# Kernel optimization log

Measured on AMD Instinct MI355X. Metric: run time of the kernel, lower is better.

The kernel has to match this reference:

```python
import jax, jax.numpy as jnp
import numpy as np

B, D, H, S = 65536, 256, 4, 64
HD = D // H  # head_dim = 64
EPS = 1e-8


def _lin(x, W, b):
    # torch nn.Linear: y = x @ W.T + b, W: [out, in]
    return x @ W.T + b


def _cos_attn(q_heads, keys, vals):
    # q_heads: [B,H,hd]; keys/vals: [H,S,hd] (shared across batch)
    qn = q_heads / (jnp.linalg.norm(q_heads, axis=-1, keepdims=True) + EPS)
    kn = keys / (jnp.linalg.norm(keys, axis=-1, keepdims=True) + EPS)
    sim = jnp.einsum('bhd,hsd->bhs', qn, kn)          # cosine sims, temp=1.0
    attn = jax.nn.softmax(sim, axis=-1)
    return jnp.einsum('bhs,hsd->bhd', attn, vals)     # [B,H,hd]


def setup_inputs() -> dict:
    key = jax.random.key(0)
    ks = jax.random.split(key, 20)

    def xavier(k, shape):
        fan_in, fan_out = shape[1], shape[0]
        lim = np.sqrt(6.0 / (fan_in + fan_out))
        return jax.random.uniform(k, shape, jnp.float32, -lim, lim)

    return {
        'query': jax.random.normal(ks[0], (B, D), jnp.float32),
        'context': jax.random.normal(ks[1], (B, D), jnp.float32),
        'fast_keys': 0.01 * jax.random.normal(ks[2], (H, S, HD), jnp.float32),
        'fast_vals': 0.01 * jax.random.normal(ks[3], (H, S, HD), jnp.float32),
        'deep_keys': 0.01 * jax.random.normal(ks[4], (H, S, HD), jnp.float32),
        'deep_vals': 0.01 * jax.random.normal(ks[5], (H, S, HD), jnp.float32),
        'Wq': xavier(ks[6], (D, D)), 'bq': jnp.zeros((D,), jnp.float32),
        'Wg': xavier(ks[7], (D, D)), 'bg': jnp.zeros((D,), jnp.float32),
        'Wc1': xavier(ks[8], (D // 2, D)), 'bc1': jnp.zeros((D // 2,), jnp.float32),
        'Wc2': xavier(ks[9], (1, D // 2)), 'bc2': jnp.zeros((1,), jnp.float32),
        'Wo': xavier(ks[10], (D, D)), 'bo': jnp.zeros((D,), jnp.float32),
        'Ws': xavier(ks[11], (D, D)), 'bs': jnp.zeros((D,), jnp.float32),
        'mix_logit': jnp.zeros((), jnp.float32),
        'surprise_mean': jnp.zeros((1, D), jnp.float32),
        'surprise_var': jnp.ones((1, D), jnp.float32),
    }


def reference(query, context, fast_keys, fast_vals, deep_keys, deep_vals,
              Wq, bq, Wg, bg, Wc1, bc1, Wc2, bc2, Wo, bo, Ws, bs,
              mix_logit, surprise_mean, surprise_var):
    # --- query projection and head split ---
    q = _lin(query, Wq, bq)                       # [B, D]
    q_heads = q.reshape(B, H, HD)                 # [B, H, hd]

    # --- dual-tier cosine-similarity attention reads ---
    v_fast = _cos_attn(q_heads, fast_keys, fast_vals).reshape(B, D)
    v_deep = _cos_attn(q_heads, deep_keys, deep_vals).reshape(B, D)

    # --- context-gated mixing of tiers ---
    gate = jnp.tanh(_lin(context, Wg, bg)).mean(axis=-1, keepdims=True)  # [B,1]
    mix = jax.nn.sigmoid(mix_logit + gate)
    out = mix * v_fast + (1.0 - mix) * v_deep

    # --- adaptive retrieval confidence head ---
    conf = jax.nn.sigmoid(_lin(jnp.tanh(_lin(context, Wc1, bc1)), Wc2, bc2))  # [B,1]
    out = out * conf
    out = _lin(out, Wo, bo)                       # [B, d_value]

    # --- surprise (detached diagnostic, does not feed output) ---
    h = jax.lax.stop_gradient(_lin(context, Ws, bs))
    z = (h - surprise_mean) / jnp.sqrt(surprise_var + 1e-6)
    surprise = jax.nn.sigmoid(jnp.abs(z).mean(axis=-1) - 2.0)  # 1/max(0.5,0.1)=2.0
    del surprise  # aux diagnostic; main output is the retrieved vector
    return out
```

## Files before the change

### kernel.cpp

```cpp
#include <hip/hip_runtime.h>

typedef unsigned short u16;
typedef __attribute__((ext_vector_type(8))) short bf16x8;
typedef __attribute__((ext_vector_type(4))) float f32x4;
typedef __attribute__((ext_vector_type(4))) unsigned short u16x4;

#define MFMA16(a, b, c) __builtin_amdgcn_mfma_f32_16x16x32_bf16((a), (b), (c), 0, 0, 0)

#define OFF_WQ   0
#define OFF_WG   65536
#define OFF_WC1  131072
#define OFF_WO   163840
#define OFF_KNF  229376
#define OFF_VTF  245760
#define OFF_KND  262144
#define OFF_VTD  278528

__device__ __forceinline__ u16 f2b(float f) {
  union { float f; unsigned u; } v; v.f = f;
  unsigned r = v.u + 0x7fffu + ((v.u >> 16) & 1u);
  return (u16)(r >> 16);
}
__device__ __forceinline__ float fsig(float x) {
  return __builtin_amdgcn_rcpf(1.f + __expf(-x));
}
__device__ __forceinline__ float ftanh(float x) {
  float e = __expf(2.f * x);
  return (e - 1.f) * __builtin_amdgcn_rcpf(e + 1.f);
}
__device__ __forceinline__ float sum16(float v) {
  v += __shfl_xor(v, 1);
  v += __shfl_xor(v, 2);
  v += __shfl_xor(v, 4);
  v += __shfl_xor(v, 8);
  return v;
}
__device__ __forceinline__ float sum64(float v) {
  v += __shfl_xor(v, 1);
  v += __shfl_xor(v, 2);
  v += __shfl_xor(v, 4);
  v += __shfl_xor(v, 8);
  v += __shfl_xor(v, 16);
  v += __shfl_xor(v, 32);
  return v;
}

__global__ void k_convert(const float* __restrict__ Wq, const float* __restrict__ Wg,
                          const float* __restrict__ Wc1, const float* __restrict__ Wo,
                          u16* __restrict__ ws) {
  int i = blockIdx.x * 256 + threadIdx.x;
  ws[OFF_WQ + i] = f2b(Wq[i]);
  ws[OFF_WG + i] = f2b(Wg[i]);
  ws[OFF_WO + i] = f2b(Wo[i]);
  if (i < 32768) ws[OFF_WC1 + i] = f2b(Wc1[i]);
}

__global__ void k_prep(const float* __restrict__ fk, const float* __restrict__ fv,
                       const float* __restrict__ dk, const float* __restrict__ dv,
                       u16* __restrict__ ws) {
  int t = blockIdx.x;
  int h = t >> 6, s = t & 63;
  int d = threadIdx.x;

  float x = fk[t * 64 + d];
  float ss = sum64(x * x);
  float sc = __builtin_amdgcn_rcpf(__builtin_amdgcn_sqrtf(ss) + 1e-8f);
  ws[OFF_KNF + t * 64 + d] = f2b(x * sc);

  x = dk[t * 64 + d];
  ss = sum64(x * x);
  sc = __builtin_amdgcn_rcpf(__builtin_amdgcn_sqrtf(ss) + 1e-8f);
  ws[OFF_KND + t * 64 + d] = f2b(x * sc);

  ws[OFF_VTF + h * 4096 + d * 64 + s] = f2b(fv[t * 64 + d]);
  ws[OFF_VTD + h * 4096 + d * 64 + s] = f2b(dv[t * 64 + d]);
}

__global__ __launch_bounds__(256, 4)
void k_fused(const float* __restrict__ query, const float* __restrict__ context,
             const float* __restrict__ bq, const float* __restrict__ bg,
             const float* __restrict__ bc1, const float* __restrict__ Wc2,
             const float* __restrict__ bc2v, const float* __restrict__ bo,
             const float* __restrict__ mixl, const u16* __restrict__ ws,
             float* __restrict__ outp) {
  __shared__ u16 sX[32 * 256];
  __shared__ float red_g[4][32];
  __shared__ float red_c[4][32];
  __shared__ float sA[32];
  __shared__ float sB[32];

  const int t = threadIdx.x;
  const int w = t >> 6;
  const int lane = t & 63;
  const int quad = lane >> 4;
  const int l16 = lane & 15;
  const int row4 = quad * 4;
  const int blk = blockIdx.x;
  char* Xb = (char*)sX;
  char* chunk = Xb + w * 4096;

  auto stage = [&](const float* src) {
    #pragma unroll
    for (int i = 0; i < 8; ++i) {
      int e = i * 1024 + t * 4;
      float4 v = *(const float4*)(src + e);
      int row = e >> 8, col = e & 255;
      u16x4 pk;
      pk.x = f2b(v.x); pk.y = f2b(v.y); pk.z = f2b(v.z); pk.w = f2b(v.w);
      *(u16x4*)(Xb + row * 512 + ((((col >> 3) ^ (row & 7)) << 4) | ((col & 7) << 1))) = pk;
    }
  };
  auto ldA = [&](int row, int kb) {
    return *(const bf16x8*)(Xb + row * 512 + ((((kb >> 3) ^ (row & 7)) << 4)));
  };
  auto ldC = [&](int row, int kb) {
    return *(const bf16x8*)(chunk + row * 128 + ((((kb >> 3) ^ (row & 7)) << 4)));
  };
  auto cwr = [&](int row, int col, u16 v) {
    *(u16*)(chunk + row * 128 + (((((col >> 3) ^ (row & 7)) << 3) | (col & 7)) << 1)) = v;
  };

  const f32x4 vzero = {0.f, 0.f, 0.f, 0.f};

  stage(context + (size_t)blk * 8192);
  __syncthreads();

  {
    f32x4 acc[2][4];
    #pragma unroll
    for (int mt = 0; mt < 2; ++mt)
      #pragma unroll
      for (int nt = 0; nt < 4; ++nt) acc[mt][nt] = vzero;
    const u16* WB = ws + OFF_WG + (w * 64 + l16) * 256;
    #pragma unroll
    for (int kk = 0; kk < 8; ++kk) {
      int kb = kk * 32 + quad * 8;
      bf16x8 a0 = ldA(l16, kb), a1 = ldA(16 + l16, kb);
      #pragma unroll
      for (int nt = 0; nt < 4; ++nt) {
        bf16x8 b = *(const bf16x8*)(WB + nt * 4096 + kb);
        acc[0][nt] = MFMA16(a0, b, acc[0][nt]);
        acc[1][nt] = MFMA16(a1, b, acc[1][nt]);
      }
    }
    float bgv[4];
    #pragma unroll
    for (int nt = 0; nt < 4; ++nt) bgv[nt] = bg[w * 64 + nt * 16 + l16];
    #pragma unroll
    for (int mt = 0; mt < 2; ++mt)
      #pragma unroll
      for (int r = 0; r < 4; ++r) {
        float s = 0.f;
        #pragma unroll
        for (int nt = 0; nt < 4; ++nt) s += ftanh(acc[mt][nt][r] + bgv[nt]);
        s = sum16(s);
        if (l16 == 0) red_g[w][mt * 16 + row4 + r] = s;
      }
  }
  {
    f32x4 acc[2][2];
    #pragma unroll
    for (int mt = 0; mt < 2; ++mt) { acc[mt][0] = vzero; acc[mt][1] = vzero; }
    const u16* WB = ws + OFF_WC1 + (w * 32 + l16) * 256;
    #pragma unroll
    for (int kk = 0; kk < 8; ++kk) {
      int kb = kk * 32 + quad * 8;
      bf16x8 a0 = ldA(l16, kb), a1 = ldA(16 + l16, kb);
      #pragma unroll
      for (int nt = 0; nt < 2; ++nt) {
        bf16x8 b = *(const bf16x8*)(WB + nt * 4096 + kb);
        acc[0][nt] = MFMA16(a0, b, acc[0][nt]);
        acc[1][nt] = MFMA16(a1, b, acc[1][nt]);
      }
    }
    float bcv[2], wcv[2];
    #pragma unroll
    for (int nt = 0; nt < 2; ++nt) {
      int n = w * 32 + nt * 16 + l16;
      bcv[nt] = bc1[n]; wcv[nt] = Wc2[n];
    }
    #pragma unroll
    for (int mt = 0; mt < 2; ++mt)
      #pragma unroll
      for (int r = 0; r < 4; ++r) {
        float s = 0.f;
        #pragma unroll
        for (int nt = 0; nt < 2; ++nt) s += ftanh(acc[mt][nt][r] + bcv[nt]) * wcv[nt];
        s = sum16(s);
        if (l16 == 0) red_c[w][mt * 16 + row4 + r] = s;
      }
  }
  __syncthreads();
  if (t < 32) {
    float g = (red_g[0][t] + red_g[1][t] + red_g[2][t] + red_g[3][t]) * (1.f / 256.f);
    float mix = fsig(mixl[0] + g);
    float conf = fsig(red_c[0][t] + red_c[1][t] + red_c[2][t] + red_c[3][t] + bc2v[0]);
    sA[t] = conf * mix;
    sB[t] = conf - conf * mix;
  }
  __syncthreads();

  stage(query + (size_t)blk * 8192);
  __syncthreads();

  f32x4 qa[2][4];
  {
    #pragma unroll
    for (int mt = 0; mt < 2; ++mt)
      #pragma unroll
      for (int nt = 0; nt < 4; ++nt) qa[mt][nt] = vzero;
    const u16* WB = ws + OFF_WQ + (w * 64 + l16) * 256;
    #pragma unroll
    for (int kk = 0; kk < 8; ++kk) {
      int kb = kk * 32 + quad * 8;
      bf16x8 a0 = ldA(l16, kb), a1 = ldA(16 + l16, kb);
      #pragma unroll
      for (int nt = 0; nt < 4; ++nt) {
        bf16x8 b = *(const bf16x8*)(WB + nt * 4096 + kb);
        qa[0][nt] = MFMA16(a0, b, qa[0][nt]);
        qa[1][nt] = MFMA16(a1, b, qa[1][nt]);
      }
    }
    float bqv[4];
    #pragma unroll
    for (int nt = 0; nt < 4; ++nt) bqv[nt] = bq[w * 64 + nt * 16 + l16];
    #pragma unroll
    for (int mt = 0; mt < 2; ++mt)
      #pragma unroll
      for (int nt = 0; nt < 4; ++nt)
        #pragma unroll
        for (int r = 0; r < 4; ++r) qa[mt][nt][r] += bqv[nt];
  }
  float scl[2][4];
  #pragma unroll
  for (int mt = 0; mt < 2; ++mt)
    #pragma unroll
    for (int r = 0; r < 4; ++r) {
      float ss = 0.f;
      #pragma unroll
      for (int nt = 0; nt < 4; ++nt) ss += qa[mt][nt][r] * qa[mt][nt][r];
      ss = sum16(ss);
      scl[mt][r] = __builtin_amdgcn_rcpf(__builtin_amdgcn_sqrtf(ss) + 1e-8f);
    }
  __syncthreads();

  #pragma unroll
  for (int mt = 0; mt < 2; ++mt)
    #pragma unroll
    for (int r = 0; r < 4; ++r) {
      int row = mt * 16 + row4 + r;
      #pragma unroll
      for (int nt = 0; nt < 4; ++nt)
        cwr(row, nt * 16 + l16, f2b(qa[mt][nt][r] * scl[mt][r]));
    }

  f32x4 sf[2][4], sd[2][4];
  #pragma unroll
  for (int mt = 0; mt < 2; ++mt)
    #pragma unroll
    for (int nt = 0; nt < 4; ++nt) { sf[mt][nt] = vzero; sd[mt][nt] = vzero; }
  {
    const u16* knF = ws + OFF_KNF + w * 4096;
    const u16* knD = ws + OFF_KND + w * 4096;
    #pragma unroll
    for (int kk = 0; kk < 2; ++kk) {
      int kb = kk * 32 + quad * 8;
      bf16x8 a0 = ldC(l16, kb), a1 = ldC(16 + l16, kb);
      #pragma unroll
      for (int nt = 0; nt < 4; ++nt) {
        bf16x8 bF = *(const bf16x8*)(knF + (nt * 16 + l16) * 64 + kb);
        bf16x8 bD = *(const bf16x8*)(knD + (nt * 16 + l16) * 64 + kb);
        sf[0][nt] = MFMA16(a0, bF, sf[0][nt]);
        sf[1][nt] = MFMA16(a1, bF, sf[1][nt]);
        sd[0][nt] = MFMA16(a0, bD, sd[0][nt]);
        sd[1][nt] = MFMA16(a1, bD, sd[1][nt]);
      }
    }
  }

  f32x4 oacc[2][4];
  {
    #pragma unroll
    for (int mt = 0; mt < 2; ++mt)
      #pragma unroll
      for (int r = 0; r < 4; ++r) {
        float rs = 0.f;
        #pragma unroll
        for (int nt = 0; nt < 4; ++nt) { float e = __expf(sf[mt][nt][r]); sf[mt][nt][r] = e; rs += e; }
        rs = sum16(rs);
        float inv = __builtin_amdgcn_rcpf(rs);
        int row = mt * 16 + row4 + r;
        #pragma unroll
        for (int nt = 0; nt < 4; ++nt) cwr(row, nt * 16 + l16, f2b(sf[mt][nt][r] * inv));
      }
    f32x4 pv[2][4];
    #pragma unroll
    for (int mt = 0; mt < 2; ++mt)
      #pragma unroll
      for (int nt = 0; nt < 4; ++nt) pv[mt][nt] = vzero;
    const u16* vT = ws + OFF_VTF + w * 4096;
    #pragma unroll
    for (int kk = 0; kk < 2; ++kk) {
      int kb = kk * 32 + quad * 8;
      bf16x8 a0 = ldC(l16, kb), a1 = ldC(16 + l16, kb);
      #pragma unroll
      for (int nt = 0; nt < 4; ++nt) {
        bf16x8 b = *(const bf16x8*)(vT + (nt * 16 + l16) * 64 + kb);
        pv[0][nt] = MFMA16(a0, b, pv[0][nt]);
        pv[1][nt] = MFMA16(a1, b, pv[1][nt]);
      }
    }
    #pragma unroll
    for (int mt = 0; mt < 2; ++mt)
      #pragma unroll
      for (int r = 0; r < 4; ++r) {
        float m_ = sA[mt * 16 + row4 + r];
        #pragma unroll
        for (int nt = 0; nt < 4; ++nt) oacc[mt][nt][r] = m_ * pv[mt][nt][r];
      }
  }
  {
    #pragma unroll
    for (int mt = 0; mt < 2; ++mt)
      #pragma unroll
      for (int r = 0; r < 4; ++r) {
        float rs = 0.f;
        #pragma unroll
        for (int nt = 0; nt < 4; ++nt) { float e = __expf(sd[mt][nt][r]); sd[mt][nt][r] = e; rs += e; }
        rs = sum16(rs);
        float inv = __builtin_amdgcn_rcpf(rs);
        int row = mt * 16 + row4 + r;
        #pragma unroll
        for (int nt = 0; nt < 4; ++nt) cwr(row, nt * 16 + l16, f2b(sd[mt][nt][r] * inv));
      }
    f32x4 pv[2][4];
    #pragma unroll
    for (int mt = 0; mt < 2; ++mt)
      #pragma unroll
      for (int nt = 0; nt < 4; ++nt) pv[mt][nt] = vzero;
    const u16* vT = ws + OFF_VTD + w * 4096;
    #pragma unroll
    for (int kk = 0; kk < 2; ++kk) {
      int kb = kk * 32 + quad * 8;
      bf16x8 a0 = ldC(l16, kb), a1 = ldC(16 + l16, kb);
      #pragma unroll
      for (int nt = 0; nt < 4; ++nt) {
        bf16x8 b = *(const bf16x8*)(vT + (nt * 16 + l16) * 64 + kb);
        pv[0][nt] = MFMA16(a0, b, pv[0][nt]);
        pv[1][nt] = MFMA16(a1, b, pv[1][nt]);
      }
    }
    #pragma unroll
    for (int mt = 0; mt < 2; ++mt)
      #pragma unroll
      for (int r = 0; r < 4; ++r) {
        float m_ = sB[mt * 16 + row4 + r];
        #pragma unroll
        for (int nt = 0; nt < 4; ++nt) oacc[mt][nt][r] += m_ * pv[mt][nt][r];
      }
  }

  __syncthreads();
  #pragma unroll
  for (int mt = 0; mt < 2; ++mt)
    #pragma unroll
    for (int r = 0; r < 4; ++r) {
      int row = mt * 16 + row4 + r;
      #pragma unroll
      for (int nt = 0; nt < 4; ++nt) {
        int col = w * 64 + nt * 16 + l16;
        *(u16*)(Xb + row * 512 + (((((col >> 3) ^ (row & 7)) << 3) | (col & 7)) << 1)) =
            f2b(oacc[mt][nt][r]);
      }
    }
  __syncthreads();

  {
    f32x4 o[2][4];
    #pragma unroll
    for (int mt = 0; mt < 2; ++mt)
      #pragma unroll
      for (int nt = 0; nt < 4; ++nt) o[mt][nt] = vzero;
    const u16* WB = ws + OFF_WO + (w * 64 + l16) * 256;
    #pragma unroll
    for (int kk = 0; kk < 8; ++kk) {
      int kb = kk * 32 + quad * 8;
      bf16x8 a0 = ldA(l16, kb), a1 = ldA(16 + l16, kb);
      #pragma unroll
      for (int nt = 0; nt < 4; ++nt) {
        bf16x8 b = *(const bf16x8*)(WB + nt * 4096 + kb);
        o[0][nt] = MFMA16(a0, b, o[0][nt]);
        o[1][nt] = MFMA16(a1, b, o[1][nt]);
      }
    }
    float bov[4];
    #pragma unroll
    for (int nt = 0; nt < 4; ++nt) bov[nt] = bo[w * 64 + nt * 16 + l16];
    float* dst = outp + (size_t)blk * 8192;
    #pragma unroll
    for (int mt = 0; mt < 2; ++mt)
      #pragma unroll
      for (int r = 0; r < 4; ++r) {
        int row = mt * 16 + row4 + r;
        #pragma unroll
        for (int nt = 0; nt < 4; ++nt)
          dst[row * 256 + w * 64 + nt * 16 + l16] = o[mt][nt][r] + bov[nt];
      }
  }
}

extern "C" void kernel_launch(void* const* d_in, const int* in_sizes, int n_in,
                              void* d_out, int out_size, void* d_ws, size_t ws_size,
                              hipStream_t stream) {
  const float* query   = (const float*)d_in[0];
  const float* context = (const float*)d_in[1];
  const float* fk      = (const float*)d_in[2];
  const float* fv      = (const float*)d_in[3];
  const float* dk      = (const float*)d_in[4];
  const float* dv      = (const float*)d_in[5];
  const float* Wq      = (const float*)d_in[6];
  const float* bq      = (const float*)d_in[7];
  const float* Wg      = (const float*)d_in[8];
  const float* bg      = (const float*)d_in[9];
  const float* Wc1     = (const float*)d_in[10];
  const float* bc1     = (const float*)d_in[11];
  const float* Wc2     = (const float*)d_in[12];
  const float* bc2     = (const float*)d_in[13];
  const float* Wo      = (const float*)d_in[14];
  const float* bo      = (const float*)d_in[15];
  const float* mixl    = (const float*)d_in[18];
  u16* ws = (u16*)d_ws;
  float* outp = (float*)d_out;

  k_convert<<<256, 256, 0, stream>>>(Wq, Wg, Wc1, Wo, ws);
  k_prep<<<256, 64, 0, stream>>>(fk, fv, dk, dv, ws);
  k_fused<<<2048, 256, 0, stream>>>(query, context, bq, bg, bc1, Wc2, bc2, bo,
                                    mixl, ws, outp);
}
```

Measured before the change: 331.7 us.

## Split fused kernel into context-gating and query-attention kernels

The single fused kernel is split into two launches. The first computes the context gate and confidence scalars per row and writes them to a workspace buffer. The second does the query projection, both attention tiers and the output projection, with separate LDS buffers for the normalized query and the probabilities. This shortens live ranges, drops one sync and interleaves the similarity computation per tier to ease register pressure. In exchange it adds a launch, a global round-trip for the scalars, and lowers k_qry's launch_bounds occupancy hint from 4 to 3.

```diff
diff --git a/kernel.cpp b/kernel.cpp
--- a/kernel.cpp
+++ b/kernel.cpp
@@ -15,6 +15,7 @@
 #define OFF_VTF  245760
 #define OFF_KND  262144
 #define OFF_VTD  278528
+#define OFF_SAB_F2 73728
 
 __device__ __forceinline__ u16 f2b(float f) {
   union { float f; unsigned u; } v; v.f = f;
@@ -77,17 +78,13 @@
 }
 
 __global__ __launch_bounds__(256, 4)
-void k_fused(const float* __restrict__ query, const float* __restrict__ context,
-             const float* __restrict__ bq, const float* __restrict__ bg,
-             const float* __restrict__ bc1, const float* __restrict__ Wc2,
-             const float* __restrict__ bc2v, const float* __restrict__ bo,
-             const float* __restrict__ mixl, const u16* __restrict__ ws,
-             float* __restrict__ outp) {
+void k_ctx(const float* __restrict__ context, const float* __restrict__ bg,
+           const float* __restrict__ bc1, const float* __restrict__ Wc2,
+           const float* __restrict__ bc2v, const float* __restrict__ mixl,
+           const u16* __restrict__ ws, float2* __restrict__ sAB) {
   __shared__ u16 sX[32 * 256];
   __shared__ float red_g[4][32];
   __shared__ float red_c[4][32];
-  __shared__ float sA[32];
-  __shared__ float sB[32];
 
   const int t = threadIdx.x;
   const int w = t >> 6;
@@ -97,9 +94,9 @@
   const int row4 = quad * 4;
   const int blk = blockIdx.x;
   char* Xb = (char*)sX;
-  char* chunk = Xb + w * 4096;
-
-  auto stage = [&](const float* src) {
+
+  {
+    const float* src = context + (size_t)blk * 8192;
     #pragma unroll
     for (int i = 0; i < 8; ++i) {
       int e = i * 1024 + t * 4;
@@ -109,21 +106,13 @@
       pk.x = f2b(v.x); pk.y = f2b(v.y); pk.z = f2b(v.z); pk.w = f2b(v.w);
       *(u16x4*)(Xb + row * 512 + ((((col >> 3) ^ (row & 7)) << 4) | ((col & 7) << 1))) = pk;
     }
-  };
+  }
+  __syncthreads();
+
   auto ldA = [&](int row, int kb) {
     return *(const bf16x8*)(Xb + row * 512 + ((((kb >> 3) ^ (row & 7)) << 4)));
   };
-  auto ldC = [&](int row, int kb) {
-    return *(const bf16x8*)(chunk + row * 128 + ((((kb >> 3) ^ (row & 7)) << 4)));
-  };
-  auto cwr = [&](int row, int col, u16 v) {
-    *(u16*)(chunk + row * 128 + (((((col >> 3) ^ (row & 7)) << 3) | (col & 7)) << 1)) = v;
-  };
-
   const f32x4 vzero = {0.f, 0.f, 0.f, 0.f};
-
-  stage(context + (size_t)blk * 8192);
-  __syncthreads();
 
   {
     f32x4 acc[2][4];
@@ -195,13 +184,65 @@
     float g = (red_g[0][t] + red_g[1][t] + red_g[2][t] + red_g[3][t]) * (1.f / 256.f);
     float mix = fsig(mixl[0] + g);
     float conf = fsig(red_c[0][t] + red_c[1][t] + red_c[2][t] + red_c[3][t] + bc2v[0]);
-    sA[t] = conf * mix;
-    sB[t] = conf - conf * mix;
-  }
-  __syncthreads();
-
-  stage(query + (size_t)blk * 8192);
-  __syncthreads();
+    sAB[(size_t)blk * 32 + t] = make_float2(conf * mix, conf - conf * mix);
+  }
+}
+
+__global__ __launch_bounds__(256, 3)
+void k_qry(const float* __restrict__ query, const float* __restrict__ bq,
+           const float* __restrict__ bo, const u16* __restrict__ ws,
+           const float2* __restrict__ sAB, float* __restrict__ outp) {
+  __shared__ u16 sX[32 * 256];
+  __shared__ u16 sY[4 * 2048];
+
+  const int t = threadIdx.x;
+  const int w = t >> 6;
+  const int lane = t & 63;
+  const int quad = lane >> 4;
+  const int l16 = lane & 15;
+  const int row4 = quad * 4;
+  const int blk = blockIdx.x;
+  char* Xb = (char*)sX;
+  char* chunkX = Xb + w * 4096;
+  char* chunkY = (char*)sY + w * 4096;
+
+  float2 ab[2][4];
+  #pragma unroll
+  for (int mt = 0; mt < 2; ++mt)
+    #pragma unroll
+    for (int r = 0; r < 4; ++r)
+      ab[mt][r] = sAB[(size_t)blk * 32 + mt * 16 + row4 + r];
+
+  {
+    const float* src = query + (size_t)blk * 8192;
+    #pragma unroll
+    for (int i = 0; i < 8; ++i) {
+      int e = i * 1024 + t * 4;
+      float4 v = *(const float4*)(src + e);
+      int row = e >> 8, col = e & 255;
+      u16x4 pk;
+      pk.x = f2b(v.x); pk.y = f2b(v.y); pk.z = f2b(v.z); pk.w = f2b(v.w);
+      *(u16x4*)(Xb + row * 512 + ((((col >> 3) ^ (row & 7)) << 4) | ((col & 7) << 1))) = pk;
+    }
+  }
+  __syncthreads();
+
+  auto ldA = [&](int row, int kb) {
+    return *(const bf16x8*)(Xb + row * 512 + ((((kb >> 3) ^ (row & 7)) << 4)));
+  };
+  auto ldX = [&](int row, int kb) {
+    return *(const bf16x8*)(chunkX + row * 128 + ((((kb >> 3) ^ (row & 7)) << 4)));
+  };
+  auto ldY = [&](int row, int kb) {
+    return *(const bf16x8*)(chunkY + row * 128 + ((((kb >> 3) ^ (row & 7)) << 4)));
+  };
+  auto xwr = [&](int row, int col, u16 v) {
+    *(u16*)(chunkX + row * 128 + (((((col >> 3) ^ (row & 7)) << 3) | (col & 7)) << 1)) = v;
+  };
+  auto ywr = [&](int row, int col, u16 v) {
+    *(u16*)(chunkY + row * 128 + (((((col >> 3) ^ (row & 7)) << 3) | (col & 7)) << 1)) = v;
+  };
+  const f32x4 vzero = {0.f, 0.f, 0.f, 0.f};
 
   f32x4 qa[2][4];
   {
@@ -231,7 +272,6 @@
         #pragma unroll
         for (int r = 0; r < 4; ++r) qa[mt][nt][r] += bqv[nt];
   }
-  float scl[2][4];
   #pragma unroll
   for (int mt = 0; mt < 2; ++mt)
     #pragma unroll
@@ -240,58 +280,46 @@
       #pragma unroll
       for (int nt = 0; nt < 4; ++nt) ss += qa[mt][nt][r] * qa[mt][nt][r];
       ss = sum16(ss);
-      scl[mt][r] = __builtin_amdgcn_rcpf(__builtin_amdgcn_sqrtf(ss) + 1e-8f);
-    }
-  __syncthreads();
-
-  #pragma unroll
-  for (int mt = 0; mt < 2; ++mt)
-    #pragma unroll
-    for (int r = 0; r < 4; ++r) {
+      float sc = __builtin_amdgcn_rcpf(__builtin_amdgcn_sqrtf(ss) + 1e-8f);
       int row = mt * 16 + row4 + r;
       #pragma unroll
       for (int nt = 0; nt < 4; ++nt)
-        cwr(row, nt * 16 + l16, f2b(qa[mt][nt][r] * scl[mt][r]));
-    }
-
-  f32x4 sf[2][4], sd[2][4];
-  #pragma unroll
-  for (int mt = 0; mt < 2; ++mt)
-    #pragma unroll
-    for (int nt = 0; nt < 4; ++nt) { sf[mt][nt] = vzero; sd[mt][nt] = vzero; }
-  {
-    const u16* knF = ws + OFF_KNF + w * 4096;
-    const u16* knD = ws + OFF_KND + w * 4096;
+        ywr(row, nt * 16 + l16, f2b(qa[mt][nt][r] * sc));
+    }
+  __syncthreads();
+
+  f32x4 oacc[2][4];
+
+  {
+    f32x4 sim[2][4];
+    #pragma unroll
+    for (int mt = 0; mt < 2; ++mt)
+      #pragma unroll
+      for (int nt = 0; nt < 4; ++nt) sim[mt][nt] = vzero;
+    const u16* kn = ws + OFF_KNF + w * 4096;
     #pragma unroll
     for (int kk = 0; kk < 2; ++kk) {
       int kb = kk * 32 + quad * 8;
-      bf16x8 a0 = ldC(l16, kb), a1 = ldC(16 + l16, kb);
-      #pragma unroll
-      for (int nt = 0; nt < 4; ++nt) {
-        bf16x8 bF = *(const bf16x8*)(knF + (nt * 16 + l16) * 64 + kb);
-        bf16x8 bD = *(const bf16x8*)(knD + (nt * 16 + l16) * 64 + kb);
-        sf[0][nt] = MFMA16(a0, bF, sf[0][nt]);
-        sf[1][nt] = MFMA16(a1, bF, sf[1][nt]);
-        sd[0][nt] = MFMA16(a0, bD, sd[0][nt]);
-        sd[1][nt] = MFMA16(a1, bD, sd[1][nt]);
-      }
-    }
-  }
-
-  f32x4 oacc[2][4];
-  {
+      bf16x8 a0 = ldY(l16, kb), a1 = ldY(16 + l16, kb);
+      #pragma unroll
+      for (int nt = 0; nt < 4; ++nt) {
+        bf16x8 b = *(const bf16x8*)(kn + (nt * 16 + l16) * 64 + kb);
+        sim[0][nt] = MFMA16(a0, b, sim[0][nt]);
+        sim[1][nt] = MFMA16(a1, b, sim[1][nt]);
+      }
+    }
     #pragma unroll
     for (int mt = 0; mt < 2; ++mt)
       #pragma unroll
       for (int r = 0; r < 4; ++r) {
         float rs = 0.f;
         #pragma unroll
-        for (int nt = 0; nt < 4; ++nt) { float e = __expf(sf[mt][nt][r]); sf[mt][nt][r] = e; rs += e; }
+        for (int nt = 0; nt < 4; ++nt) { float e = __expf(sim[mt][nt][r]); sim[mt][nt][r] = e; rs += e; }
         rs = sum16(rs);
         float inv = __builtin_amdgcn_rcpf(rs);
         int row = mt * 16 + row4 + r;
         #pragma unroll
-        for (int nt = 0; nt < 4; ++nt) cwr(row, nt * 16 + l16, f2b(sf[mt][nt][r] * inv));
+        for (int nt = 0; nt < 4; ++nt) xwr(row, nt * 16 + l16, f2b(sim[mt][nt][r] * inv));
       }
     f32x4 pv[2][4];
     #pragma unroll
@@ -302,7 +330,7 @@
     #pragma unroll
     for (int kk = 0; kk < 2; ++kk) {
       int kb = kk * 32 + quad * 8;
-      bf16x8 a0 = ldC(l16, kb), a1 = ldC(16 + l16, kb);
+      bf16x8 a0 = ldX(l16, kb), a1 = ldX(16 + l16, kb);
       #pragma unroll
       for (int nt = 0; nt < 4; ++nt) {
         bf16x8 b = *(const bf16x8*)(vT + (nt * 16 + l16) * 64 + kb);
@@ -314,24 +342,41 @@
     for (int mt = 0; mt < 2; ++mt)
       #pragma unroll
       for (int r = 0; r < 4; ++r) {
-        float m_ = sA[mt * 16 + row4 + r];
+        float m_ = ab[mt][r].x;
         #pragma unroll
         for (int nt = 0; nt < 4; ++nt) oacc[mt][nt][r] = m_ * pv[mt][nt][r];
       }
   }
   {
+    f32x4 sim[2][4];
+    #pragma unroll
+    for (int mt = 0; mt < 2; ++mt)
+      #pragma unroll
+      for (int nt = 0; nt < 4; ++nt) sim[mt][nt] = vzero;
+    const u16* kn = ws + OFF_KND + w * 4096;
+    #pragma unroll
+    for (int kk = 0; kk < 2; ++kk) {
+      int kb = kk * 32 + quad * 8;
+      bf16x8 a0 = ldY(l16, kb), a1 = ldY(16 + l16, kb);
+      #pragma unroll
+      for (int nt = 0; nt < 4; ++nt) {
+        bf16x8 b = *(const bf16x8*)(kn + (nt * 16 + l16) * 64 + kb);
+        sim[0][nt] = MFMA16(a0, b, sim[0][nt]);
+        sim[1][nt] = MFMA16(a1, b, sim[1][nt]);
+      }
+    }
     #pragma unroll
     for (int mt = 0; mt < 2; ++mt)
       #pragma unroll
       for (int r = 0; r < 4; ++r) {
         float rs = 0.f;
         #pragma unroll
-        for (int nt = 0; nt < 4; ++nt) { float e = __expf(sd[mt][nt][r]); sd[mt][nt][r] = e; rs += e; }
+        for (int nt = 0; nt < 4; ++nt) { float e = __expf(sim[mt][nt][r]); sim[mt][nt][r] = e; rs += e; }
         rs = sum16(rs);
         float inv = __builtin_amdgcn_rcpf(rs);
         int row = mt * 16 + row4 + r;
         #pragma unroll
-        for (int nt = 0; nt < 4; ++nt) cwr(row, nt * 16 + l16, f2b(sd[mt][nt][r] * inv));
+        for (int nt = 0; nt < 4; ++nt) xwr(row, nt * 16 + l16, f2b(sim[mt][nt][r] * inv));
       }
     f32x4 pv[2][4];
     #pragma unroll
@@ -342,7 +387,7 @@
     #pragma unroll
     for (int kk = 0; kk < 2; ++kk) {
       int kb = kk * 32 + quad * 8;
-      bf16x8 a0 = ldC(l16, kb), a1 = ldC(16 + l16, kb);
+      bf16x8 a0 = ldX(l16, kb), a1 = ldX(16 + l16, kb);
       #pragma unroll
       for (int nt = 0; nt < 4; ++nt) {
         bf16x8 b = *(const bf16x8*)(vT + (nt * 16 + l16) * 64 + kb);
@@ -354,7 +399,7 @@
     for (int mt = 0; mt < 2; ++mt)
       #pragma unroll
       for (int r = 0; r < 4; ++r) {
-        float m_ = sB[mt * 16 + row4 + r];
+        float m_ = ab[mt][r].y;
         #pragma unroll
         for (int nt = 0; nt < 4; ++nt) oacc[mt][nt][r] += m_ * pv[mt][nt][r];
       }
@@ -430,10 +475,11 @@
   const float* bo      = (const float*)d_in[15];
   const float* mixl    = (const float*)d_in[18];
   u16* ws = (u16*)d_ws;
+  float2* sAB = (float2*)((char*)d_ws + 589824);
   float* outp = (float*)d_out;
 
   k_convert<<<256, 256, 0, stream>>>(Wq, Wg, Wc1, Wo, ws);
   k_prep<<<256, 64, 0, stream>>>(fk, fv, dk, dv, ws);
-  k_fused<<<2048, 256, 0, stream>>>(query, context, bq, bg, bc1, Wc2, bc2, bo,
-                                    mixl, ws, outp);
-}
+  k_ctx<<<2048, 256, 0, stream>>>(context, bg, bc1, Wc2, bc2, mixl, ws, sAB);
+  k_qry<<<2048, 256, 0, stream>>>(query, bq, bo, ws, sAB, outp);
+}
```

Result: slower. 347.8 us (+4.8%).

## Give each wave its own 16 rows and drop block-level syncs

Applied to the files above, without the earlier changes.

Restructures the fused kernel so each wave owns 16 full rows end to end instead of a block sharing 32 rows split by output columns. A-fragments load straight from global memory into registers with bf16 conversion, skipping the shared-memory staging, and cross-wave reductions and __syncthreads become wave barriers. This removes block-wide synchronisation and LDS traffic for the inputs. In exchange each wave reads the full weight matrices, so weight traffic per row rises, and the larger register footprint lowers the launch bound to 3 blocks per CU.

```diff
diff --git a/kernel.cpp b/kernel.cpp
--- a/kernel.cpp
+++ b/kernel.cpp
@@ -3,7 +3,6 @@
 typedef unsigned short u16;
 typedef __attribute__((ext_vector_type(8))) short bf16x8;
 typedef __attribute__((ext_vector_type(4))) float f32x4;
-typedef __attribute__((ext_vector_type(4))) unsigned short u16x4;
 
 #define MFMA16(a, b, c) __builtin_amdgcn_mfma_f32_16x16x32_bf16((a), (b), (c), 0, 0, 0)
 
@@ -36,10 +35,7 @@
   return v;
 }
 __device__ __forceinline__ float sum64(float v) {
-  v += __shfl_xor(v, 1);
-  v += __shfl_xor(v, 2);
-  v += __shfl_xor(v, 4);
-  v += __shfl_xor(v, 8);
+  v = sum16(v);
   v += __shfl_xor(v, 16);
   v += __shfl_xor(v, 32);
   return v;
@@ -76,336 +72,242 @@
   ws[OFF_VTD + h * 4096 + d * 64 + s] = f2b(dv[t * 64 + d]);
 }
 
-__global__ __launch_bounds__(256, 4)
-void k_fused(const float* __restrict__ query, const float* __restrict__ context,
-             const float* __restrict__ bq, const float* __restrict__ bg,
-             const float* __restrict__ bc1, const float* __restrict__ Wc2,
-             const float* __restrict__ bc2v, const float* __restrict__ bo,
-             const float* __restrict__ mixl, const u16* __restrict__ ws,
-             float* __restrict__ outp) {
-  __shared__ u16 sX[32 * 256];
-  __shared__ float red_g[4][32];
-  __shared__ float red_c[4][32];
-  __shared__ float sA[32];
-  __shared__ float sB[32];
+__global__ __launch_bounds__(256, 3)
+void k_main(const float* __restrict__ query, const float* __restrict__ context,
+            const float* __restrict__ bq, const float* __restrict__ bg,
+            const float* __restrict__ bc1, const float* __restrict__ Wc2,
+            const float* __restrict__ bc2v, const float* __restrict__ bo,
+            const float* __restrict__ mixl, const u16* __restrict__ ws,
+            float* __restrict__ outp) {
+  __shared__ u16 sQ[4][16 * 256];
+  __shared__ u16 sP[4][16 * 64];
 
   const int t = threadIdx.x;
   const int w = t >> 6;
   const int lane = t & 63;
   const int quad = lane >> 4;
   const int l16 = lane & 15;
-  const int row4 = quad * 4;
-  const int blk = blockIdx.x;
-  char* Xb = (char*)sX;
-  char* chunk = Xb + w * 4096;
-
-  auto stage = [&](const float* src) {
-    #pragma unroll
-    for (int i = 0; i < 8; ++i) {
-      int e = i * 1024 + t * 4;
-      float4 v = *(const float4*)(src + e);
-      int row = e >> 8, col = e & 255;
-      u16x4 pk;
-      pk.x = f2b(v.x); pk.y = f2b(v.y); pk.z = f2b(v.z); pk.w = f2b(v.w);
-      *(u16x4*)(Xb + row * 512 + ((((col >> 3) ^ (row & 7)) << 4) | ((col & 7) << 1))) = pk;
+  const int row0 = (blockIdx.x * 4 + w) * 16;
+  char* Q = (char*)sQ[w];
+  char* P = (char*)sP[w];
+
+  const f32x4 vzero = {0.f, 0.f, 0.f, 0.f};
+
+  auto load_frags = [&](const float* __restrict__ src, bf16x8* fr) {
+    const float* p = src + (size_t)(row0 + l16) * 256 + quad * 8;
+    #pragma unroll
+    for (int kk = 0; kk < 8; ++kk) {
+      float4 v0 = *(const float4*)(p + kk * 32);
+      float4 v1 = *(const float4*)(p + kk * 32 + 4);
+      bf16x8 a;
+      a[0] = (short)f2b(v0.x); a[1] = (short)f2b(v0.y);
+      a[2] = (short)f2b(v0.z); a[3] = (short)f2b(v0.w);
+      a[4] = (short)f2b(v1.x); a[5] = (short)f2b(v1.y);
+      a[6] = (short)f2b(v1.z); a[7] = (short)f2b(v1.w);
+      fr[kk] = a;
     }
   };
-  auto ldA = [&](int row, int kb) {
-    return *(const bf16x8*)(Xb + row * 512 + ((((kb >> 3) ^ (row & 7)) << 4)));
-  };
-  auto ldC = [&](int row, int kb) {
-    return *(const bf16x8*)(chunk + row * 128 + ((((kb >> 3) ^ (row & 7)) << 4)));
-  };
-  auto cwr = [&](int row, int col, u16 v) {
-    *(u16*)(chunk + row * 128 + (((((col >> 3) ^ (row & 7)) << 3) | (col & 7)) << 1)) = v;
-  };
-
-  const f32x4 vzero = {0.f, 0.f, 0.f, 0.f};
-
-  stage(context + (size_t)blk * 8192);
-  __syncthreads();
-
+
+  bf16x8 fr[8];
+  float abx[4], aby[4];
+
+  load_frags(context, fr);
   {
-    f32x4 acc[2][4];
-    #pragma unroll
-    for (int mt = 0; mt < 2; ++mt)
-      #pragma unroll
-      for (int nt = 0; nt < 4; ++nt) acc[mt][nt] = vzero;
-    const u16* WB = ws + OFF_WG + (w * 64 + l16) * 256;
-    #pragma unroll
-    for (int kk = 0; kk < 8; ++kk) {
-      int kb = kk * 32 + quad * 8;
-      bf16x8 a0 = ldA(l16, kb), a1 = ldA(16 + l16, kb);
+    f32x4 acc[16];
+    #pragma unroll
+    for (int nt = 0; nt < 16; ++nt) acc[nt] = vzero;
+    const u16* WB = ws + OFF_WG + l16 * 256;
+    #pragma unroll
+    for (int nt = 0; nt < 16; ++nt)
+      #pragma unroll
+      for (int kk = 0; kk < 8; ++kk) {
+        bf16x8 b = *(const bf16x8*)(WB + nt * 4096 + kk * 32 + quad * 8);
+        acc[nt] = MFMA16(fr[kk], b, acc[nt]);
+      }
+    float gate_r[4];
+    #pragma unroll
+    for (int r = 0; r < 4; ++r) {
+      float s = 0.f;
+      #pragma unroll
+      for (int nt = 0; nt < 16; ++nt) s += ftanh(acc[nt][r] + bg[nt * 16 + l16]);
+      gate_r[r] = sum16(s) * (1.f / 256.f);
+    }
+    f32x4 cacc[8];
+    #pragma unroll
+    for (int nt = 0; nt < 8; ++nt) cacc[nt] = vzero;
+    const u16* WC = ws + OFF_WC1 + l16 * 256;
+    #pragma unroll
+    for (int nt = 0; nt < 8; ++nt)
+      #pragma unroll
+      for (int kk = 0; kk < 8; ++kk) {
+        bf16x8 b = *(const bf16x8*)(WC + nt * 4096 + kk * 32 + quad * 8);
+        cacc[nt] = MFMA16(fr[kk], b, cacc[nt]);
+      }
+    float ml = mixl[0], b2 = bc2v[0];
+    #pragma unroll
+    for (int r = 0; r < 4; ++r) {
+      float s = 0.f;
+      #pragma unroll
+      for (int nt = 0; nt < 8; ++nt)
+        s += ftanh(cacc[nt][r] + bc1[nt * 16 + l16]) * Wc2[nt * 16 + l16];
+      float conf = fsig(sum16(s) + b2);
+      float mix = fsig(ml + gate_r[r]);
+      abx[r] = conf * mix;
+      aby[r] = conf - conf * mix;
+    }
+  }
+
+  load_frags(query, fr);
+  {
+    f32x4 q[16];
+    #pragma unroll
+    for (int nt = 0; nt < 16; ++nt) q[nt] = vzero;
+    const u16* WB = ws + OFF_WQ + l16 * 256;
+    #pragma unroll
+    for (int nt = 0; nt < 16; ++nt)
+      #pragma unroll
+      for (int kk = 0; kk < 8; ++kk) {
+        bf16x8 b = *(const bf16x8*)(WB + nt * 4096 + kk * 32 + quad * 8);
+        q[nt] = MFMA16(fr[kk], b, q[nt]);
+      }
+    #pragma unroll
+    for (int nt = 0; nt < 16; ++nt) {
+      float bv = bq[nt * 16 + l16];
+      #pragma unroll
+      for (int r = 0; r < 4; ++r) q[nt][r] += bv;
+    }
+    #pragma unroll
+    for (int h = 0; h < 4; ++h) {
+      float sc[4];
+      #pragma unroll
+      for (int r = 0; r < 4; ++r) {
+        float ss = 0.f;
+        #pragma unroll
+        for (int j = 0; j < 4; ++j) { float x = q[h * 4 + j][r]; ss += x * x; }
+        ss = sum16(ss);
+        sc[r] = __builtin_amdgcn_rcpf(__builtin_amdgcn_sqrtf(ss) + 1e-8f);
+      }
+      #pragma unroll
+      for (int j = 0; j < 4; ++j) {
+        int nt = h * 4 + j;
+        int col = nt * 16 + l16;
+        #pragma unroll
+        for (int r = 0; r < 4; ++r) {
+          int row = quad * 4 + r;
+          *(u16*)(Q + row * 512 + (((((col >> 3) ^ (row & 7)) << 3) | (col & 7)) << 1)) =
+              f2b(q[nt][r] * sc[r]);
+        }
+      }
+    }
+  }
+  __builtin_amdgcn_wave_barrier();
+
+  f32x4 o16[16];
+  #pragma unroll
+  for (int h = 0; h < 4; ++h) {
+    bf16x8 qf[2];
+    #pragma unroll
+    for (int kk = 0; kk < 2; ++kk) {
+      int col = h * 64 + kk * 32 + quad * 8;
+      qf[kk] = *(const bf16x8*)(Q + l16 * 512 + ((((col >> 3) ^ (l16 & 7)) << 4)));
+    }
+    #pragma unroll
+    for (int tier = 0; tier < 2; ++tier) {
+      const u16* kn = ws + (tier ? OFF_KND : OFF_KNF) + h * 4096;
+      const u16* vt = ws + (tier ? OFF_VTD : OFF_VTF) + h * 4096;
+      f32x4 sim[4];
       #pragma unroll
       for (int nt = 0; nt < 4; ++nt) {
-        bf16x8 b = *(const bf16x8*)(WB + nt * 4096 + kb);
-        acc[0][nt] = MFMA16(a0, b, acc[0][nt]);
-        acc[1][nt] = MFMA16(a1, b, acc[1][nt]);
-      }
-    }
-    float bgv[4];
-    #pragma unroll
-    for (int nt = 0; nt < 4; ++nt) bgv[nt] = bg[w * 64 + nt * 16 + l16];
-    #pragma unroll
-    for (int mt = 0; mt < 2; ++mt)
-      #pragma unroll
-      for (int r = 0; r < 4; ++r) {
-        float s = 0.f;
-        #pragma unroll
-        for (int nt = 0; nt < 4; ++nt) s += ftanh(acc[mt][nt][r] + bgv[nt]);
-        s = sum16(s);
-        if (l16 == 0) red_g[w][mt * 16 + row4 + r] = s;
-      }
-  }
-  {
-    f32x4 acc[2][2];
-    #pragma unroll
-    for (int mt = 0; mt < 2; ++mt) { acc[mt][0] = vzero; acc[mt][1] = vzero; }
-    const u16* WB = ws + OFF_WC1 + (w * 32 + l16) * 256;
-    #pragma unroll
-    for (int kk = 0; kk < 8; ++kk) {
-      int kb = kk * 32 + quad * 8;
-      bf16x8 a0 = ldA(l16, kb), a1 = ldA(16 + l16, kb);
-      #pragma unroll
-      for (int nt = 0; nt < 2; ++nt) {
-        bf16x8 b = *(const bf16x8*)(WB + nt * 4096 + kb);
-        acc[0][nt] = MFMA16(a0, b, acc[0][nt]);
-        acc[1][nt] = MFMA16(a1, b, acc[1][nt]);
-      }
-    }
-    float bcv[2], wcv[2];
-    #pragma unroll
-    for (int nt = 0; nt < 2; ++nt) {
-      int n = w * 32 + nt * 16 + l16;
-      bcv[nt] = bc1[n]; wcv[nt] = Wc2[n];
-    }
-    #pragma unroll
-    for (int mt = 0; mt < 2; ++mt)
-      #pragma unroll
-      for (int r = 0; r < 4; ++r) {
-        float s = 0.f;
-        #pragma unroll
-        for (int nt = 0; nt < 2; ++nt) s += ftanh(acc[mt][nt][r] + bcv[nt]) * wcv[nt];
-        s = sum16(s);
-        if (l16 == 0) red_c[w][mt * 16 + row4 + r] = s;
-      }
-  }
-  __syncthreads();
-  if (t < 32) {
-    float g = (red_g[0][t] + red_g[1][t] + red_g[2][t] + red_g[3][t]) * (1.f / 256.f);
-    float mix = fsig(mixl[0] + g);
-    float conf = fsig(red_c[0][t] + red_c[1][t] + red_c[2][t] + red_c[3][t] + bc2v[0]);
-    sA[t] = conf * mix;
-    sB[t] = conf - conf * mix;
-  }
-  __syncthreads();
-
-  stage(query + (size_t)blk * 8192);
-  __syncthreads();
-
-  f32x4 qa[2][4];
-  {
-    #pragma unroll
-    for (int mt = 0; mt < 2; ++mt)
-      #pragma unroll
-      for (int nt = 0; nt < 4; ++nt) qa[mt][nt] = vzero;
-    const u16* WB = ws + OFF_WQ + (w * 64 + l16) * 256;
-    #pragma unroll
-    for (int kk = 0; kk < 8; ++kk) {
-      int kb = kk * 32 + quad * 8;
-      bf16x8 a0 = ldA(l16, kb), a1 = ldA(16 + l16, kb);
-      #pragma unroll
-      for (int nt = 0; nt < 4; ++nt) {
-        bf16x8 b = *(const bf16x8*)(WB + nt * 4096 + kb);
-        qa[0][nt] = MFMA16(a0, b, qa[0][nt]);
-        qa[1][nt] = MFMA16(a1, b, qa[1][nt]);
-      }
-    }
-    float bqv[4];
-    #pragma unroll
-    for (int nt = 0; nt < 4; ++nt) bqv[nt] = bq[w * 64 + nt * 16 + l16];
-    #pragma unroll
-    for (int mt = 0; mt < 2; ++mt)
-      #pragma unroll
-      for (int nt = 0; nt < 4; ++nt)
-        #pragma unroll
-        for (int r = 0; r < 4; ++r) qa[mt][nt][r] += bqv[nt];
-  }
-  float scl[2][4];
-  #pragma unroll
-  for (int mt = 0; mt < 2; ++mt)
-    #pragma unroll
-    for (int r = 0; r < 4; ++r) {
-      float ss = 0.f;
-      #pragma unroll
-      for (int nt = 0; nt < 4; ++nt) ss += qa[mt][nt][r] * qa[mt][nt][r];
-      ss = sum16(ss);
-      scl[mt][r] = __builtin_amdgcn_rcpf(__builtin_amdgcn_sqrtf(ss) + 1e-8f);
-    }
-  __syncthreads();
-
-  #pragma unroll
-  for (int mt = 0; mt < 2; ++mt)
-    #pragma unroll
-    for (int r = 0; r < 4; ++r) {
-      int row = mt * 16 + row4 + r;
-      #pragma unroll
-      for (int nt = 0; nt < 4; ++nt)
-        cwr(row, nt * 16 + l16, f2b(qa[mt][nt][r] * scl[mt][r]));
-    }
-
-  f32x4 sf[2][4], sd[2][4];
-  #pragma unroll
-  for (int mt = 0; mt < 2; ++mt)
-    #pragma unroll
-    for (int nt = 0; nt < 4; ++nt) { sf[mt][nt] = vzero; sd[mt][nt] = vzero; }
-  {
-    const u16* knF = ws + OFF_KNF + w * 4096;
-    const u16* knD = ws + OFF_KND + w * 4096;
-    #pragma unroll
-    for (int kk = 0; kk < 2; ++kk) {
-      int kb = kk * 32 + quad * 8;
-      bf16x8 a0 = ldC(l16, kb), a1 = ldC(16 + l16, kb);
-      #pragma unroll
-      for (int nt = 0; nt < 4; ++nt) {
-        bf16x8 bF = *(const bf16x8*)(knF + (nt * 16 + l16) * 64 + kb);
-        bf16x8 bD = *(const bf16x8*)(knD + (nt * 16 + l16) * 64 + kb);
-        sf[0][nt] = MFMA16(a0, bF, sf[0][nt]);
-        sf[1][nt] = MFMA16(a1, bF, sf[1][nt]);
-        sd[0][nt] = MFMA16(a0, bD, sd[0][nt]);
-        sd[1][nt] = MFMA16(a1, bD, sd[1][nt]);
-      }
-    }
-  }
-
-  f32x4 oacc[2][4];
-  {
-    #pragma unroll
-    for (int mt = 0; mt < 2; ++mt)
+        sim[nt] = vzero;
+        #pragma unroll
+        for (int kk = 0; kk < 2; ++kk) {
+          bf16x8 b = *(const bf16x8*)(kn + (nt * 16 + l16) * 64 + kk * 32 + quad * 8);
+          sim[nt] = MFMA16(qf[kk], b, sim[nt]);
+        }
+      }
       #pragma unroll
       for (int r = 0; r < 4; ++r) {
         float rs = 0.f;
         #pragma unroll
-        for (int nt = 0; nt < 4; ++nt) { float e = __expf(sf[mt][nt][r]); sf[mt][nt][r] = e; rs += e; }
+        for (int nt = 0; nt < 4; ++nt) {
+          float e = __expf(sim[nt][r]); sim[nt][r] = e; rs += e;
+        }
         rs = sum16(rs);
         float inv = __builtin_amdgcn_rcpf(rs);
-        int row = mt * 16 + row4 + r;
-        #pragma unroll
-        for (int nt = 0; nt < 4; ++nt) cwr(row, nt * 16 + l16, f2b(sf[mt][nt][r] * inv));
-      }
-    f32x4 pv[2][4];
-    #pragma unroll
-    for (int mt = 0; mt < 2; ++mt)
-      #pragma unroll
-      for (int nt = 0; nt < 4; ++nt) pv[mt][nt] = vzero;
-    const u16* vT = ws + OFF_VTF + w * 4096;
-    #pragma unroll
-    for (int kk = 0; kk < 2; ++kk) {
-      int kb = kk * 32 + quad * 8;
-      bf16x8 a0 = ldC(l16, kb), a1 = ldC(16 + l16, kb);
+        int row = quad * 4 + r;
+        #pragma unroll
+        for (int nt = 0; nt < 4; ++nt) {
+          int col = nt * 16 + l16;
+          *(u16*)(P + row * 128 + (((((col >> 3) ^ (row & 7)) << 3) | (col & 7)) << 1)) =
+              f2b(sim[nt][r] * inv);
+        }
+      }
+      __builtin_amdgcn_wave_barrier();
+      bf16x8 pf[2];
+      #pragma unroll
+      for (int kk = 0; kk < 2; ++kk) {
+        int col = kk * 32 + quad * 8;
+        pf[kk] = *(const bf16x8*)(P + l16 * 128 + ((((col >> 3) ^ (l16 & 7)) << 4)));
+      }
+      f32x4 pv[4];
       #pragma unroll
       for (int nt = 0; nt < 4; ++nt) {
-        bf16x8 b = *(const bf16x8*)(vT + (nt * 16 + l16) * 64 + kb);
-        pv[0][nt] = MFMA16(a0, b, pv[0][nt]);
-        pv[1][nt] = MFMA16(a1, b, pv[1][nt]);
-      }
-    }
-    #pragma unroll
-    for (int mt = 0; mt < 2; ++mt)
+        pv[nt] = vzero;
+        #pragma unroll
+        for (int kk = 0; kk < 2; ++kk) {
+          bf16x8 b = *(const bf16x8*)(vt + (nt * 16 + l16) * 64 + kk * 32 + quad * 8);
+          pv[nt] = MFMA16(pf[kk], b, pv[nt]);
+        }
+      }
+      #pragma unroll
+      for (int nt = 0; nt < 4; ++nt)
+        #pragma unroll
+        for (int r = 0; r < 4; ++r) {
+          float m_ = tier ? aby[r] : abx[r];
+          if (tier == 0) o16[h * 4 + nt][r] = m_ * pv[nt][r];
+          else           o16[h * 4 + nt][r] += m_ * pv[nt][r];
+        }
+      __builtin_amdgcn_wave_barrier();
+    }
+  }
+
+  #pragma unroll
+  for (int nt = 0; nt < 16; ++nt) {
+    int col = nt * 16 + l16;
+    #pragma unroll
+    for (int r = 0; r < 4; ++r) {
+      int row = quad * 4 + r;
+      *(u16*)(Q + row * 512 + (((((col >> 3) ^ (row & 7)) << 3) | (col & 7)) << 1)) =
+          f2b(o16[nt][r]);
+    }
+  }
+  __builtin_amdgcn_wave_barrier();
+  #pragma unroll
+  for (int kk = 0; kk < 8; ++kk) {
+    int col = kk * 32 + quad * 8;
+    fr[kk] = *(const bf16x8*)(Q + l16 * 512 + ((((col >> 3) ^ (l16 & 7)) << 4)));
+  }
+  {
+    f32x4 o[16];
+    #pragma unroll
+    for (int nt = 0; nt < 16; ++nt) o[nt] = vzero;
+    const u16* WB = ws + OFF_WO + l16 * 256;
+    #pragma unroll
+    for (int nt = 0; nt < 16; ++nt)
+      #pragma unroll
+      for (int kk = 0; kk < 8; ++kk) {
+        bf16x8 b = *(const bf16x8*)(WB + nt * 4096 + kk * 32 + quad * 8);
+        o[nt] = MFMA16(fr[kk], b, o[nt]);
+      }
+    #pragma unroll
+    for (int nt = 0; nt < 16; ++nt) {
+      float bv = bo[nt * 16 + l16];
       #pragma unroll
       for (int r = 0; r < 4; ++r) {
-        float m_ = sA[mt * 16 + row4 + r];
-        #pragma unroll
-        for (int nt = 0; nt < 4; ++nt) oacc[mt][nt][r] = m_ * pv[mt][nt][r];
-      }
-  }
-  {
-    #pragma unroll
-    for (int mt = 0; mt < 2; ++mt)
-      #pragma unroll
-      for (int r = 0; r < 4; ++r) {
-        float rs = 0.f;
-        #pragma unroll
-        for (int nt = 0; nt < 4; ++nt) { float e = __expf(sd[mt][nt][r]); sd[mt][nt][r] = e; rs += e; }
-        rs = sum16(rs);
-        float inv = __builtin_amdgcn_rcpf(rs);
-        int row = mt * 16 + row4 + r;
-        #pragma unroll
-        for (int nt = 0; nt < 4; ++nt) cwr(row, nt * 16 + l16, f2b(sd[mt][nt][r] * inv));
-      }
-    f32x4 pv[2][4];
-    #pragma unroll
-    for (int mt = 0; mt < 2; ++mt)
-      #pragma unroll
-      for (int nt = 0; nt < 4; ++nt) pv[mt][nt] = vzero;
-    const u16* vT = ws + OFF_VTD + w * 4096;
-    #pragma unroll
-    for (int kk = 0; kk < 2; ++kk) {
-      int kb = kk * 32 + quad * 8;
-      bf16x8 a0 = ldC(l16, kb), a1 = ldC(16 + l16, kb);
-      #pragma unroll
-      for (int nt = 0; nt < 4; ++nt) {
-        bf16x8 b = *(const bf16x8*)(vT + (nt * 16 + l16) * 64 + kb);
-        pv[0][nt] = MFMA16(a0, b, pv[0][nt]);
-        pv[1][nt] = MFMA16(a1, b, pv[1][nt]);
-      }
-    }
-    #pragma unroll
-    for (int mt = 0; mt < 2; ++mt)
-      #pragma unroll
-      for (int r = 0; r < 4; ++r) {
-        float m_ = sB[mt * 16 + row4 + r];
-        #pragma unroll
-        for (int nt = 0; nt < 4; ++nt) oacc[mt][nt][r] += m_ * pv[mt][nt][r];
-      }
-  }
-
-  __syncthreads();
-  #pragma unroll
-  for (int mt = 0; mt < 2; ++mt)
-    #pragma unroll
-    for (int r = 0; r < 4; ++r) {
-      int row = mt * 16 + row4 + r;
-      #pragma unroll
-      for (int nt = 0; nt < 4; ++nt) {
-        int col = w * 64 + nt * 16 + l16;
-        *(u16*)(Xb + row * 512 + (((((col >> 3) ^ (row & 7)) << 3) | (col & 7)) << 1)) =
-            f2b(oacc[mt][nt][r]);
-      }
-    }
-  __syncthreads();
-
-  {
-    f32x4 o[2][4];
-    #pragma unroll
-    for (int mt = 0; mt < 2; ++mt)
-      #pragma unroll
-      for (int nt = 0; nt < 4; ++nt) o[mt][nt] = vzero;
-    const u16* WB = ws + OFF_WO + (w * 64 + l16) * 256;
-    #pragma unroll
-    for (int kk = 0; kk < 8; ++kk) {
-      int kb = kk * 32 + quad * 8;
-      bf16x8 a0 = ldA(l16, kb), a1 = ldA(16 + l16, kb);
-      #pragma unroll
-      for (int nt = 0; nt < 4; ++nt) {
-        bf16x8 b = *(const bf16x8*)(WB + nt * 4096 + kb);
-        o[0][nt] = MFMA16(a0, b, o[0][nt]);
-        o[1][nt] = MFMA16(a1, b, o[1][nt]);
-      }
-    }
-    float bov[4];
-    #pragma unroll
-    for (int nt = 0; nt < 4; ++nt) bov[nt] = bo[w * 64 + nt * 16 + l16];
-    float* dst = outp + (size_t)blk * 8192;
-    #pragma unroll
-    for (int mt = 0; mt < 2; ++mt)
-      #pragma unroll
-      for (int r = 0; r < 4; ++r) {
-        int row = mt * 16 + row4 + r;
-        #pragma unroll
-        for (int nt = 0; nt < 4; ++nt)
-          dst[row * 256 + w * 64 + nt * 16 + l16] = o[mt][nt][r] + bov[nt];
-      }
+        int row = row0 + quad * 4 + r;
+        outp[(size_t)row * 256 + nt * 16 + l16] = o[nt][r] + bv;
+      }
+    }
   }
 }
 
@@ -434,6 +336,6 @@
 
   k_convert<<<256, 256, 0, stream>>>(Wq, Wg, Wc1, Wo, ws);
   k_prep<<<256, 64, 0, stream>>>(fk, fv, dk, dv, ws);
-  k_fused<<<2048, 256, 0, stream>>>(query, context, bq, bg, bc1, Wc2, bc2, bo,
-                                    mixl, ws, outp);
-}
+  k_main<<<1024, 256, 0, stream>>>(query, context, bq, bg, bc1, Wc2, bc2, bo,
+                                   mixl, ws, outp);
+}
```

Result: slower. 659.7 us (+98.9%).
